# Optimization experiments

Measured on AMD Instinct MI355X. Metric: run time of the kernel, lower is better.

Reference implementation:

```python
import jax, jax.numpy as jnp
import numpy as np

NUM_EXPERTS = 4
HIDDEN = 768
INTER = 192  # expert_inter; gate_up projects to 2*INTER
TOKENS = 131072


def setup_inputs() -> dict:
    key = jax.random.key(0)
    k1, k2, k3, k4 = jax.random.split(key, 4)
    hidden = jax.random.normal(k1, (TOKENS, HIDDEN), dtype=jnp.float32)
    expert_ids = jax.random.randint(k2, (TOKENS,), 0, NUM_EXPERTS, dtype=jnp.int64)
    gate_up = jax.random.normal(k3, (NUM_EXPERTS, HIDDEN, 2 * INTER), dtype=jnp.float32) * 0.02
    down = jax.random.normal(k4, (NUM_EXPERTS, INTER, HIDDEN), dtype=jnp.float32) * 0.02
    return {"hidden": hidden, "expert_ids": expert_ids, "gate_up": gate_up, "down": down}


def reference(hidden, expert_ids, gate_up, down):
    # Math-equivalent to scatter -> per-expert SwiGLU MLP -> gather back:
    # for each token t with expert e = expert_ids[t]:
    #   out[t] = (silu(x_t @ gate_up[e][:, :F]) * (x_t @ gate_up[e][:, F:])) @ down[e]
    # With E=4 (small), compute per-expert dense and select via one-hot; this is
    # jit-friendly (static shapes) and exactly matches the per-token math.
    E = gate_up.shape[0]
    F = down.shape[1]
    onehot = (expert_ids[None, :] == jnp.arange(E)[:, None]).astype(hidden.dtype)  # [E, T]
    gu = jnp.einsum('th,ehf->etf', hidden, gate_up)      # [E, T, 2F]
    gate, up = gu[..., :F], gu[..., F:]                  # [E, T, F]
    act = jax.nn.silu(gate) * up                         # SwiGLU
    out = jnp.einsum('etf,efh,et->th', act, down, onehot)  # select token's own expert
    return out
```

## Files before the change

### kernel.cpp

```cpp
#include <hip/hip_runtime.h>
#include <hip/hip_bf16.h>

#define NE 4
#define HD 768
#define F2 384
#define F1 192
#define NT 131072
#define TT 128

typedef __attribute__((ext_vector_type(8))) short bf16x8;
typedef __attribute__((ext_vector_type(4))) float f32x4;
typedef __attribute__((ext_vector_type(4))) unsigned int u32x4;

#define SMEM_BYTES 73984
#define LTOK 73728u

#define WS_BUCKET_OFF 256
#define WS_B1IMG_OFF (WS_BUCKET_OFF + NE*NT*4)
#define WS_DNIMG_OFF (WS_B1IMG_OFF + NE*24*24576)

__device__ __forceinline__ unsigned short f2bf(float x) {
    unsigned int u = __float_as_uint(x);
    return (unsigned short)((u + 0x7fffu + ((u >> 16) & 1u)) >> 16);
}
__device__ __forceinline__ unsigned int pk2(float a, float b) {
    unsigned int ua = __float_as_uint(a), ub = __float_as_uint(b);
    unsigned int lo = (ua + 0x7fffu + ((ua >> 16) & 1u)) >> 16;
    unsigned int hi = (ub + 0x7fffu + ((ub >> 16) & 1u)) & 0xffff0000u;
    return lo | hi;
}
#define GLL(srcp, ldsoff) \
    __builtin_amdgcn_global_load_lds((const __attribute__((address_space(1))) void*)(srcp), \
        (__attribute__((address_space(3))) void*)(smem + (ldsoff)), 16, 0, 0)

__global__ void route_kernel(const int* __restrict__ ids, int* __restrict__ counts,
                             int* __restrict__ bucket) {
    __shared__ int lc[NE];
    __shared__ int lb[NE];
    int tid = threadIdx.x;
    if (tid < NE) lc[tid] = 0;
    __syncthreads();
    int t = blockIdx.x * blockDim.x + tid;
    int e = ids[t];
    int rank = atomicAdd(&lc[e], 1);
    __syncthreads();
    if (tid < NE) lb[tid] = atomicAdd(&counts[tid], lc[tid]);
    __syncthreads();
    bucket[e * NT + lb[e] + rank] = t;
}

__global__ void b1img_kernel(const float* __restrict__ gu, unsigned short* __restrict__ b1img) {
    int idx = blockIdx.x * 256 + threadIdx.x;
    int L = idx % 1536;
    int es = idx / 1536;
    int kstep = es % 24, e = es / 24;
    int colp = L >> 3, slot = L & 7;
    int v = slot ^ (colp & 7);
    int tc = colp * 2 + (v >> 2);
    int kb = kstep * 32 + (v & 3) * 8;
    const float* src = gu + ((size_t)(e * HD + kb)) * F2 + tc;
    unsigned short o[8];
    #pragma unroll
    for (int j = 0; j < 8; ++j) o[j] = f2bf(src[(size_t)j * F2]);
    *(bf16x8*)(b1img + ((size_t)idx) * 8) = *(const bf16x8*)o;
}

__global__ void dnimg_kernel(const float* __restrict__ dn, unsigned short* __restrict__ dnimg) {
    int idx = blockIdx.x * 256 + threadIdx.x;
    int L = idx % 1536;
    int r = idx / 1536;
    int kt = r % 6; r /= 6;
    int half = r & 1; int e = r >> 1;
    int colp = L >> 3, slot = L & 7;
    int v = slot ^ (colp & 7);
    int tc = colp * 2 + (v >> 2);
    int kb = kt * 32 + (v & 3) * 8;
    const float* src = dn + ((size_t)(e * F1 + kb)) * HD + half * 384 + tc;
    unsigned short o[8];
    #pragma unroll
    for (int j = 0; j < 8; ++j) o[j] = f2bf(src[(size_t)j * HD]);
    *(bf16x8*)(dnimg + ((size_t)idx) * 8) = *(const bf16x8*)o;
}

__global__ __launch_bounds__(512, 2)
void moe_kernel(const float* __restrict__ hidden, const int* __restrict__ counts,
                const int* __restrict__ bucket, const unsigned short* __restrict__ b1img,
                const unsigned short* __restrict__ dnimg, float* __restrict__ out)
{
    extern __shared__ __align__(16) unsigned char smem[];
    const unsigned LAo[2] = {0u, 8192u};
    const unsigned LBo[2] = {16384u, 40960u};
    const unsigned LB2 = 49152u;
    const unsigned LACT = 0u;

    int rem = blockIdx.x, e, n_e = 0;
    for (e = 0; e < NE; ++e) {
        n_e = counts[e];
        int ntiles = (n_e + TT - 1) >> 7;
        if (rem < ntiles) break;
        rem -= ntiles;
    }
    if (e >= NE) return;
    int t0 = rem << 7;

    int tid = threadIdx.x;
    int lane = tid & 63;
    int w = tid >> 6;
    int rw64 = (w >> 2) << 6;
    int cq = w & 3;
    int lg = lane >> 4;
    int l16 = lane & 15;

    int* tokp = (int*)(smem + LTOK);
    if (tid < TT) {
        int idx = t0 + tid; if (idx >= n_e) idx = n_e - 1;
        tokp[tid] = bucket[e * NT + idx];
    }
    __syncthreads();

    int arow = tid >> 2, kq = tid & 3;
    const float* aptr = hidden + (size_t)tokp[arow] * HD + kq * 8;
    unsigned awb = (unsigned)((tid >> 3) * 128 +
                   (((kq + ((arow & 1) << 2)) ^ ((tid >> 3) & 7)) << 4));

    const unsigned short* gls  = b1img + (size_t)e * 24 * 12288 + (w * 3) * 512 + lane * 8;
    const unsigned short* gls2 = dnimg + (size_t)e * 12 * 12288 + (w * 3) * 512 + lane * 8;
    unsigned gld = (unsigned)(w * 3) * 1024u;

    unsigned laneoff = (unsigned)(((l16 >> 1) << 7) +
                       (((lg + ((l16 & 1) << 2)) ^ (l16 >> 1)) << 4));
    unsigned arb[4], brb[6], b2rb[6];
    #pragma unroll
    for (int mt = 0; mt < 4; ++mt)
        arb[mt] = (unsigned)((rw64 + mt * 16) * 64) + laneoff;
    #pragma unroll
    for (int nt = 0; nt < 6; ++nt) {
        int tcb = (nt < 3) ? (cq * 48 + nt * 16) : (192 + cq * 48 + (nt - 3) * 16);
        brb[nt] = (unsigned)(tcb * 64) + laneoff;
        b2rb[nt] = LB2 + (unsigned)((cq * 96 + nt * 16) * 64) + laneoff;
    }

    f32x4 avb[4][2];
    const f32x4 fzero = {0.f, 0.f, 0.f, 0.f};
    f32x4 acc[4][6];
    #pragma unroll
    for (int mt = 0; mt < 4; ++mt)
        #pragma unroll
        for (int nt = 0; nt < 6; ++nt) acc[mt][nt] = fzero;

    {
        #pragma unroll
        for (int i = 0; i < 3; ++i) GLL(gls + i * 512, LBo[0] + gld + i * 1024u);
        #pragma unroll
        for (int j = 0; j < 4; ++j) {
            const f32x4* p = (const f32x4*)(aptr + j * 32);
            avb[j][0] = p[0]; avb[j][1] = p[1];
        }
        u32x4 vv = {pk2(avb[0][0].x,avb[0][0].y), pk2(avb[0][0].z,avb[0][0].w),
                    pk2(avb[0][1].x,avb[0][1].y), pk2(avb[0][1].z,avb[0][1].w)};
        *(u32x4*)(smem + LAo[0] + awb) = vv;
        asm volatile("s_waitcnt vmcnt(3) lgkmcnt(0)");
        __builtin_amdgcn_s_barrier();
        __builtin_amdgcn_sched_barrier(0);
    }

    #pragma unroll
    for (int g = 0; g < 24; ++g) {
        if (g < 23) {
            #pragma unroll
            for (int i = 0; i < 3; ++i)
                GLL(gls + (size_t)(g + 1) * 12288 + i * 512, LBo[(g + 1) & 1] + gld + i * 1024u);
        }
        if (g < 20) {
            const f32x4* p = (const f32x4*)(aptr + (g + 4) * 32);
            avb[g & 3][0] = p[0]; avb[g & 3][1] = p[1];
        }

        bf16x8 Af[4];
        #pragma unroll
        for (int mt = 0; mt < 4; ++mt)
            Af[mt] = *(const bf16x8*)(smem + LAo[g & 1] + arb[mt]);
        __builtin_amdgcn_s_setprio(1);
        #pragma unroll
        for (int nt = 0; nt < 6; ++nt) {
            bf16x8 Bf = *(const bf16x8*)(smem + LBo[g & 1] + brb[nt]);
            #pragma unroll
            for (int mt = 0; mt < 4; ++mt)
                acc[mt][nt] = __builtin_amdgcn_mfma_f32_16x16x32_bf16(Af[mt], Bf, acc[mt][nt], 0, 0, 0);
        }
        __builtin_amdgcn_s_setprio(0);

        if (g < 23) {
            f32x4 a0 = avb[(g + 1) & 3][0], a1 = avb[(g + 1) & 3][1];
            u32x4 vv = {pk2(a0.x,a0.y), pk2(a0.z,a0.w), pk2(a1.x,a1.y), pk2(a1.z,a1.w)};
            *(u32x4*)(smem + LAo[(g + 1) & 1] + awb) = vv;
            if (g < 20) asm volatile("s_waitcnt vmcnt(1) lgkmcnt(0)");
            else        asm volatile("s_waitcnt vmcnt(0) lgkmcnt(0)");
            __builtin_amdgcn_s_barrier();
            __builtin_amdgcn_sched_barrier(0);
        }
    }

    asm volatile("s_waitcnt vmcnt(0) lgkmcnt(0)");
    __builtin_amdgcn_s_barrier();
    __builtin_amdgcn_sched_barrier(0);

    #pragma unroll
    for (int i = 0; i < 3; ++i) GLL(gls2 + i * 512, LB2 + gld + i * 1024u);

    #pragma unroll
    for (int mt = 0; mt < 4; ++mt)
        #pragma unroll
        for (int nt = 0; nt < 3; ++nt)
            #pragma unroll
            for (int p = 0; p < 4; ++p) {
                float g = acc[mt][nt][p];
                float u = acc[mt][nt + 3][p];
                float s = g / (1.f + __expf(-g));
                int row = rw64 + mt * 16 + 4 * lg + p;
                int f = cq * 48 + nt * 16 + l16;
                int c = f >> 3;
                unsigned b = (unsigned)(LACT + row * 384 + (((c & 24) | ((c & 7) ^ (row & 7))) << 4) + (f & 7) * 2);
                *(unsigned short*)(smem + b) = f2bf(s * u);
            }
    asm volatile("s_waitcnt vmcnt(0) lgkmcnt(0)");
    __builtin_amdgcn_s_barrier();
    __builtin_amdgcn_sched_barrier(0);

    #pragma unroll
    for (int half = 0; half < 2; ++half) {
        f32x4 c2[4][6];
        #pragma unroll
        for (int mt = 0; mt < 4; ++mt)
            #pragma unroll
            for (int nt = 0; nt < 6; ++nt) c2[mt][nt] = fzero;

        #pragma unroll
        for (int kt = 0; kt < 6; ++kt) {
            const int s = half * 6 + kt;

            int c = kt * 4 + lg;
            unsigned a2sl = (unsigned)(((c & 24) | ((c & 7) ^ (l16 & 7))) << 4);
            bf16x8 A2[4], B2f[6];
            #pragma unroll
            for (int mt = 0; mt < 4; ++mt)
                A2[mt] = *(const bf16x8*)(smem + LACT + (rw64 + mt * 16 + l16) * 384 + a2sl);
            #pragma unroll
            for (int nt = 0; nt < 6; ++nt)
                B2f[nt] = *(const bf16x8*)(smem + b2rb[nt]);
            asm volatile("s_waitcnt lgkmcnt(0)");
            __builtin_amdgcn_s_barrier();
            __builtin_amdgcn_sched_barrier(0);

            if (s < 11) {
                #pragma unroll
                for (int i = 0; i < 3; ++i)
                    GLL(gls2 + (size_t)(s + 1) * 12288 + i * 512, LB2 + gld + i * 1024u);
            }

            __builtin_amdgcn_s_setprio(1);
            #pragma unroll
            for (int nt = 0; nt < 6; ++nt)
                #pragma unroll
                for (int mt = 0; mt < 4; ++mt)
                    c2[mt][nt] = __builtin_amdgcn_mfma_f32_16x16x32_bf16(A2[mt], B2f[nt], c2[mt][nt], 0, 0, 0);
            __builtin_amdgcn_s_setprio(0);

            if (s < 11) {
                asm volatile("s_waitcnt vmcnt(0)");
                __builtin_amdgcn_s_barrier();
                __builtin_amdgcn_sched_barrier(0);
            }
        }

        #pragma unroll
        for (int mt = 0; mt < 4; ++mt)
            #pragma unroll
            for (int p = 0; p < 4; ++p) {
                int row = rw64 + mt * 16 + 4 * lg + p;
                if (t0 + row < n_e) {
                    float* orow = out + (size_t)tokp[row] * HD + half * 384 + cq * 96 + l16;
                    #pragma unroll
                    for (int nt = 0; nt < 6; ++nt)
                        orow[nt * 16] = c2[mt][nt][p];
                }
            }
    }
}

extern "C" void kernel_launch(void* const* d_in, const int* in_sizes, int n_in,
                              void* d_out, int out_size, void* d_ws, size_t ws_size,
                              hipStream_t stream) {
    (void)in_sizes; (void)n_in; (void)out_size; (void)ws_size;
    const float* hidden = (const float*)d_in[0];
    const int*   ids    = (const int*)d_in[1];
    const float* gu     = (const float*)d_in[2];
    const float* dn     = (const float*)d_in[3];
    float* out = (float*)d_out;

    char* ws = (char*)d_ws;
    int* counts = (int*)ws;
    int* bucket = (int*)(ws + WS_BUCKET_OFF);
    unsigned short* b1img = (unsigned short*)(ws + WS_B1IMG_OFF);
    unsigned short* dnimg = (unsigned short*)(ws + WS_DNIMG_OFF);

    hipMemsetAsync(d_ws, 0, 64, stream);
    route_kernel<<<NT / 256, 256, 0, stream>>>(ids, counts, bucket);
    b1img_kernel<<<576, 256, 0, stream>>>(gu, b1img);
    dnimg_kernel<<<288, 256, 0, stream>>>(dn, dnimg);
    moe_kernel<<<1028, 512, SMEM_BYTES, stream>>>(hidden, counts, bucket, b1img, dnimg, out);
}
```

Before: 310.1 us.

## Double K-step per stage with larger double-buffered LDS tiles at one block per CU

Restructures both GEMM phases to process two 32-wide K slices per pipeline stage, halving the number of barriers and waits. Shared memory grows to about 148KB with separate double buffers for A, B1 and the down-projection tiles, so launch bounds drop to one 512-thread block per CU. The down-projection loads now prefetch a full stage ahead instead of single-buffered per-step loads. Losing the second resident block reduces latency hiding across blocks, and the full vmcnt(0) waits may expose memory latency.

```diff
diff --git a/kernel.cpp b/kernel.cpp
--- a/kernel.cpp
+++ b/kernel.cpp
@@ -12,8 +12,15 @@
 typedef __attribute__((ext_vector_type(4))) float f32x4;
 typedef __attribute__((ext_vector_type(4))) unsigned int u32x4;
 
-#define SMEM_BYTES 73984
-#define LTOK 73728u
+#define LA0 0u
+#define LA1 16384u
+#define LB0 32768u
+#define LB1 81920u
+#define LACT 0u
+#define LC0 49152u
+#define LC1 98304u
+#define LTOK 147456u
+#define SMEM_BYTES 147968
 
 #define WS_BUCKET_OFF 256
 #define WS_B1IMG_OFF (WS_BUCKET_OFF + NE*NT*4)
@@ -82,16 +89,12 @@
     *(bf16x8*)(dnimg + ((size_t)idx) * 8) = *(const bf16x8*)o;
 }
 
-__global__ __launch_bounds__(512, 2)
+__global__ __launch_bounds__(512, 1)
 void moe_kernel(const float* __restrict__ hidden, const int* __restrict__ counts,
                 const int* __restrict__ bucket, const unsigned short* __restrict__ b1img,
                 const unsigned short* __restrict__ dnimg, float* __restrict__ out)
 {
     extern __shared__ __align__(16) unsigned char smem[];
-    const unsigned LAo[2] = {0u, 8192u};
-    const unsigned LBo[2] = {16384u, 40960u};
-    const unsigned LB2 = 49152u;
-    const unsigned LACT = 0u;
 
     int rem = blockIdx.x, e, n_e = 0;
     for (e = 0; e < NE; ++e) {
@@ -119,12 +122,14 @@
     __syncthreads();
 
     int arow = tid >> 2, kq = tid & 3;
-    const float* aptr = hidden + (size_t)tokp[arow] * HD + kq * 8;
-    unsigned awb = (unsigned)((tid >> 3) * 128 +
-                   (((kq + ((arow & 1) << 2)) ^ ((tid >> 3) & 7)) << 4));
-
-    const unsigned short* gls  = b1img + (size_t)e * 24 * 12288 + (w * 3) * 512 + lane * 8;
-    const unsigned short* gls2 = dnimg + (size_t)e * 12 * 12288 + (w * 3) * 512 + lane * 8;
+    const float* aptr = hidden + (size_t)tokp[arow] * HD + kq * 16;
+    unsigned awb0 = (unsigned)(arow * 128 + (((2 * kq)     ^ (arow & 7)) << 4));
+    unsigned awb1 = (unsigned)(arow * 128 + (((2 * kq + 1) ^ (arow & 7)) << 4));
+
+    const unsigned char* g1 = (const unsigned char*)b1img + (size_t)e * 589824
+                              + (w * 3) * 1024 + lane * 16;
+    const unsigned char* g2 = (const unsigned char*)dnimg + (size_t)e * 294912
+                              + (w * 3) * 1024 + lane * 16;
     unsigned gld = (unsigned)(w * 3) * 1024u;
 
     unsigned laneoff = (unsigned)(((l16 >> 1) << 7) +
@@ -132,15 +137,45 @@
     unsigned arb[4], brb[6], b2rb[6];
     #pragma unroll
     for (int mt = 0; mt < 4; ++mt)
-        arb[mt] = (unsigned)((rw64 + mt * 16) * 64) + laneoff;
+        arb[mt] = (unsigned)((rw64 + mt * 16 + l16) * 128);
     #pragma unroll
     for (int nt = 0; nt < 6; ++nt) {
         int tcb = (nt < 3) ? (cq * 48 + nt * 16) : (192 + cq * 48 + (nt - 3) * 16);
         brb[nt] = (unsigned)(tcb * 64) + laneoff;
-        b2rb[nt] = LB2 + (unsigned)((cq * 96 + nt * 16) * 64) + laneoff;
-    }
-
-    f32x4 avb[4][2];
+        b2rb[nt] = (unsigned)((cq * 96 + nt * 16) * 64) + laneoff;
+    }
+    unsigned xk0 = (unsigned)((lg ^ (l16 & 7)) << 4);
+    unsigned xk1 = (unsigned)(((4 + lg) ^ (l16 & 7)) << 4);
+
+    f32x4 av[4];
+    auto issueA = [&](int g) {
+        const f32x4* p = (const f32x4*)(aptr + g * 64);
+        av[0] = p[0]; av[1] = p[1]; av[2] = p[2]; av[3] = p[3];
+    };
+    auto writeA = [&](unsigned base) {
+        u32x4 lo = {pk2(av[0].x,av[0].y), pk2(av[0].z,av[0].w), pk2(av[1].x,av[1].y), pk2(av[1].z,av[1].w)};
+        u32x4 hi = {pk2(av[2].x,av[2].y), pk2(av[2].z,av[2].w), pk2(av[3].x,av[3].y), pk2(av[3].z,av[3].w)};
+        *(u32x4*)(smem + base + awb0) = lo;
+        *(u32x4*)(smem + base + awb1) = hi;
+    };
+    auto gllB1 = [&](int g, unsigned dstbase) {
+        #pragma unroll
+        for (int j = 0; j < 2; ++j)
+            #pragma unroll
+            for (int i = 0; i < 3; ++i)
+                GLL(g1 + (size_t)(2 * g + j) * 24576 + i * 1024,
+                    dstbase + (unsigned)j * 24576u + gld + i * 1024u);
+    };
+    auto gllB2 = [&](int q, unsigned dstbase) {
+        int h = q / 3, s = q % 3;
+        #pragma unroll
+        for (int j = 0; j < 2; ++j)
+            #pragma unroll
+            for (int i = 0; i < 3; ++i)
+                GLL(g2 + (size_t)(h * 6 + 2 * s + j) * 24576 + i * 1024,
+                    dstbase + (unsigned)j * 24576u + gld + i * 1024u);
+    };
+
     const f32x4 fzero = {0.f, 0.f, 0.f, 0.f};
     f32x4 acc[4][6];
     #pragma unroll
@@ -148,66 +183,52 @@
         #pragma unroll
         for (int nt = 0; nt < 6; ++nt) acc[mt][nt] = fzero;
 
-    {
-        #pragma unroll
-        for (int i = 0; i < 3; ++i) GLL(gls + i * 512, LBo[0] + gld + i * 1024u);
-        #pragma unroll
-        for (int j = 0; j < 4; ++j) {
-            const f32x4* p = (const f32x4*)(aptr + j * 32);
-            avb[j][0] = p[0]; avb[j][1] = p[1];
+    issueA(0);
+    gllB1(0, LB0);
+    writeA(LA0);
+    asm volatile("s_waitcnt vmcnt(0) lgkmcnt(0)");
+    __builtin_amdgcn_s_barrier();
+    __builtin_amdgcn_sched_barrier(0);
+
+    #pragma unroll 1
+    for (int g = 0; g < 12; ++g) {
+        unsigned Ab  = (g & 1) ? LA1 : LA0;
+        unsigned Bb  = (g & 1) ? LB1 : LB0;
+        unsigned Abn = (g & 1) ? LA0 : LA1;
+        unsigned Bbn = (g & 1) ? LB0 : LB1;
+        if (g < 11) { issueA(g + 1); gllB1(g + 1, Bbn); }
+
+        #pragma unroll
+        for (int kk = 0; kk < 2; ++kk) {
+            unsigned xk = kk ? xk1 : xk0;
+            unsigned bsub = Bb + (unsigned)kk * 24576u;
+            bf16x8 Af[4], Bf[6];
+            #pragma unroll
+            for (int mt = 0; mt < 4; ++mt) Af[mt] = *(const bf16x8*)(smem + Ab + arb[mt] + xk);
+            #pragma unroll
+            for (int nt = 0; nt < 6; ++nt) Bf[nt] = *(const bf16x8*)(smem + bsub + brb[nt]);
+            __builtin_amdgcn_s_setprio(1);
+            #pragma unroll
+            for (int nt = 0; nt < 6; ++nt)
+                #pragma unroll
+                for (int mt = 0; mt < 4; ++mt)
+                    acc[mt][nt] = __builtin_amdgcn_mfma_f32_16x16x32_bf16(Af[mt], Bf[nt], acc[mt][nt], 0, 0, 0);
+            __builtin_amdgcn_s_setprio(0);
         }
-        u32x4 vv = {pk2(avb[0][0].x,avb[0][0].y), pk2(avb[0][0].z,avb[0][0].w),
-                    pk2(avb[0][1].x,avb[0][1].y), pk2(avb[0][1].z,avb[0][1].w)};
-        *(u32x4*)(smem + LAo[0] + awb) = vv;
-        asm volatile("s_waitcnt vmcnt(3) lgkmcnt(0)");
-        __builtin_amdgcn_s_barrier();
-        __builtin_amdgcn_sched_barrier(0);
-    }
-
-    #pragma unroll
-    for (int g = 0; g < 24; ++g) {
-        if (g < 23) {
-            #pragma unroll
-            for (int i = 0; i < 3; ++i)
-                GLL(gls + (size_t)(g + 1) * 12288 + i * 512, LBo[(g + 1) & 1] + gld + i * 1024u);
-        }
-        if (g < 20) {
-            const f32x4* p = (const f32x4*)(aptr + (g + 4) * 32);
-            avb[g & 3][0] = p[0]; avb[g & 3][1] = p[1];
-        }
-
-        bf16x8 Af[4];
-        #pragma unroll
-        for (int mt = 0; mt < 4; ++mt)
-            Af[mt] = *(const bf16x8*)(smem + LAo[g & 1] + arb[mt]);
-        __builtin_amdgcn_s_setprio(1);
-        #pragma unroll
-        for (int nt = 0; nt < 6; ++nt) {
-            bf16x8 Bf = *(const bf16x8*)(smem + LBo[g & 1] + brb[nt]);
-            #pragma unroll
-            for (int mt = 0; mt < 4; ++mt)
-                acc[mt][nt] = __builtin_amdgcn_mfma_f32_16x16x32_bf16(Af[mt], Bf, acc[mt][nt], 0, 0, 0);
-        }
-        __builtin_amdgcn_s_setprio(0);
-
-        if (g < 23) {
-            f32x4 a0 = avb[(g + 1) & 3][0], a1 = avb[(g + 1) & 3][1];
-            u32x4 vv = {pk2(a0.x,a0.y), pk2(a0.z,a0.w), pk2(a1.x,a1.y), pk2(a1.z,a1.w)};
-            *(u32x4*)(smem + LAo[(g + 1) & 1] + awb) = vv;
-            if (g < 20) asm volatile("s_waitcnt vmcnt(1) lgkmcnt(0)");
-            else        asm volatile("s_waitcnt vmcnt(0) lgkmcnt(0)");
+
+        if (g < 11) {
+            writeA(Abn);
+            asm volatile("s_waitcnt vmcnt(0) lgkmcnt(0)");
             __builtin_amdgcn_s_barrier();
             __builtin_amdgcn_sched_barrier(0);
         }
     }
 
-    asm volatile("s_waitcnt vmcnt(0) lgkmcnt(0)");
+    asm volatile("s_waitcnt lgkmcnt(0)");
     __builtin_amdgcn_s_barrier();
     __builtin_amdgcn_sched_barrier(0);
 
-    #pragma unroll
-    for (int i = 0; i < 3; ++i) GLL(gls2 + i * 512, LB2 + gld + i * 1024u);
-
+    gllB2(0, LC0);
     #pragma unroll
     for (int mt = 0; mt < 4; ++mt)
         #pragma unroll
@@ -236,38 +257,34 @@
             for (int nt = 0; nt < 6; ++nt) c2[mt][nt] = fzero;
 
         #pragma unroll
-        for (int kt = 0; kt < 6; ++kt) {
-            const int s = half * 6 + kt;
-
-            int c = kt * 4 + lg;
-            unsigned a2sl = (unsigned)(((c & 24) | ((c & 7) ^ (l16 & 7))) << 4);
-            bf16x8 A2[4], B2f[6];
-            #pragma unroll
-            for (int mt = 0; mt < 4; ++mt)
-                A2[mt] = *(const bf16x8*)(smem + LACT + (rw64 + mt * 16 + l16) * 384 + a2sl);
-            #pragma unroll
-            for (int nt = 0; nt < 6; ++nt)
-                B2f[nt] = *(const bf16x8*)(smem + b2rb[nt]);
-            asm volatile("s_waitcnt lgkmcnt(0)");
-            __builtin_amdgcn_s_barrier();
-            __builtin_amdgcn_sched_barrier(0);
-
-            if (s < 11) {
-                #pragma unroll
-                for (int i = 0; i < 3; ++i)
-                    GLL(gls2 + (size_t)(s + 1) * 12288 + i * 512, LB2 + gld + i * 1024u);
-            }
-
-            __builtin_amdgcn_s_setprio(1);
-            #pragma unroll
-            for (int nt = 0; nt < 6; ++nt)
+        for (int s = 0; s < 3; ++s) {
+            const int q = half * 3 + s;
+            unsigned Cb = (q & 1) ? LC1 : LC0;
+            if (q < 5) gllB2(q + 1, (q & 1) ? LC0 : LC1);
+
+            #pragma unroll
+            for (int kk = 0; kk < 2; ++kk) {
+                int c = s * 8 + kk * 4 + lg;
+                unsigned a2sl = (unsigned)(((c & 24) | ((c & 7) ^ (l16 & 7))) << 4);
+                unsigned bsub = Cb + (unsigned)kk * 24576u;
+                bf16x8 A2[4], B2f[6];
                 #pragma unroll
                 for (int mt = 0; mt < 4; ++mt)
-                    c2[mt][nt] = __builtin_amdgcn_mfma_f32_16x16x32_bf16(A2[mt], B2f[nt], c2[mt][nt], 0, 0, 0);
-            __builtin_amdgcn_s_setprio(0);
-
-            if (s < 11) {
-                asm volatile("s_waitcnt vmcnt(0)");
+                    A2[mt] = *(const bf16x8*)(smem + LACT + (rw64 + mt * 16 + l16) * 384 + a2sl);
+                #pragma unroll
+                for (int nt = 0; nt < 6; ++nt)
+                    B2f[nt] = *(const bf16x8*)(smem + bsub + b2rb[nt]);
+                __builtin_amdgcn_s_setprio(1);
+                #pragma unroll
+                for (int nt = 0; nt < 6; ++nt)
+                    #pragma unroll
+                    for (int mt = 0; mt < 4; ++mt)
+                        c2[mt][nt] = __builtin_amdgcn_mfma_f32_16x16x32_bf16(A2[mt], B2f[nt], c2[mt][nt], 0, 0, 0);
+                __builtin_amdgcn_s_setprio(0);
+            }
+
+            if (q < 5) {
+                asm volatile("s_waitcnt vmcnt(0) lgkmcnt(0)");
                 __builtin_amdgcn_s_barrier();
                 __builtin_amdgcn_sched_barrier(0);
             }
```

Result: faster. 292.4 us (-5.7%).
